# Kernel tuning notes

Measured on AMD Instinct MI355X. Metric: run time of the kernel, lower is better.

## Reference

```python
import jax, jax.numpy as jnp
import numpy as np

B, S, E, H = 2, 2048, 1024, 16
D = E // H  # head_dim = 64


def setup_inputs() -> dict:
    key = jax.random.key(0)
    ks = jax.random.split(key, 11)
    s = 1.0 / np.sqrt(E)
    return {
        "query": jax.random.normal(ks[0], (B, S, E), jnp.float32),
        "key":   jax.random.normal(ks[1], (B, S, E), jnp.float32),
        "value": jax.random.normal(ks[2], (B, S, E), jnp.float32),
        "q_w": jax.random.uniform(ks[3], (E, E), jnp.float32, -s, s),
        "q_b": jax.random.uniform(ks[4], (E,), jnp.float32, -s, s),
        "k_w": jax.random.uniform(ks[5], (E, E), jnp.float32, -s, s),
        "k_b": jax.random.uniform(ks[6], (E,), jnp.float32, -s, s),
        "v_w": jax.random.uniform(ks[7], (E, E), jnp.float32, -s, s),
        "v_b": jax.random.uniform(ks[8], (E,), jnp.float32, -s, s),
        "o_w": jax.random.uniform(ks[9], (E, E), jnp.float32, -s, s),
        "o_b": jax.random.uniform(ks[10], (E,), jnp.float32, -s, s),
    }


def reference(query, key, value, q_w, q_b, k_w, k_b, v_w, v_b, o_w, o_b):
    b, sq, _ = query.shape
    sk = key.shape[1]
    # linear projections (torch Linear: x @ W.T + b)
    Q = (query @ q_w.T + q_b).reshape(b, sq, H, D).transpose(0, 2, 1, 3)  # b h sq d
    K = (key   @ k_w.T + k_b).reshape(b, sk, H, D).transpose(0, 2, 1, 3)
    V = (value @ v_w.T + v_b).reshape(b, sk, H, D).transpose(0, 2, 1, 3)
    scores = jnp.einsum("bhqd,bhkd->bhqk", Q, K) / jnp.sqrt(jnp.float32(D))
    attn = jax.nn.softmax(scores, axis=-1)
    out = jnp.einsum("bhqk,bhkd->bhqd", attn, V)  # b h sq d
    out = out.transpose(0, 2, 1, 3).reshape(b, sq, E)
    return out @ o_w.T + o_b
```

## Files before the change

kernel.cpp:

```cpp
#include <hip/hip_runtime.h>
#include <stdint.h>

typedef __bf16 bf16x8 __attribute__((ext_vector_type(8)));
typedef short short8 __attribute__((ext_vector_type(8)));
typedef float f32x4 __attribute__((ext_vector_type(4)));
typedef float f32x16 __attribute__((ext_vector_type(16)));
typedef unsigned short u16;
typedef unsigned int u32;

#define MROWS 4096
#define EDIM  1024
#define SQ    2048
#define DH    64

#if __has_builtin(__builtin_amdgcn_exp2f)
#define EXP2(x) __builtin_amdgcn_exp2f(x)
#else
#define EXP2(x) exp2f(x)
#endif

__device__ __forceinline__ u16 f2bf(float f) {
  unsigned u = __builtin_bit_cast(unsigned, f);
  return (u16)((u + 0x7FFFu + ((u >> 16) & 1u)) >> 16);
}

__device__ __forceinline__ u32 cvtpk_bf16(float lo, float hi) {
  u32 r;
  asm("v_cvt_pk_bf16_f32 %0, %1, %2" : "=v"(r) : "v"(lo), "v"(hi));
  return r;
}
__device__ __forceinline__ void swap32(u32& a, u32& b) {
  asm("v_permlane32_swap_b32 %0, %1" : "+v"(a), "+v"(b));
}

__global__ __launch_bounds__(256) void cvt7_kernel(
    const float* __restrict__ s0, const float* __restrict__ s1,
    const float* __restrict__ s2, const float* __restrict__ s3,
    const float* __restrict__ s4, const float* __restrict__ s5,
    const float* __restrict__ s6,
    u16* __restrict__ d0, u16* __restrict__ d1, u16* __restrict__ d2,
    u16* __restrict__ d3, u16* __restrict__ d4, u16* __restrict__ d5,
    u16* __restrict__ d6, int nact, int nw) {
  const float* s; u16* d; int n;
  switch (blockIdx.y) {
    case 0: s = s0; d = d0; n = nact; break;
    case 1: s = s1; d = d1; n = nact; break;
    case 2: s = s2; d = d2; n = nact; break;
    case 3: s = s3; d = d3; n = nw; break;
    case 4: s = s4; d = d4; n = nw; break;
    case 5: s = s5; d = d5; n = nw; break;
    default: s = s6; d = d6; n = nw; break;
  }
  int i = (blockIdx.x * 256 + threadIdx.x) * 8;
  if (i >= n) return;
  float4 a = *(const float4*)(s + i);
  float4 b = *(const float4*)(s + i + 4);
  short8 r;
  r[0] = (short)f2bf(a.x); r[1] = (short)f2bf(a.y);
  r[2] = (short)f2bf(a.z); r[3] = (short)f2bf(a.w);
  r[4] = (short)f2bf(b.x); r[5] = (short)f2bf(b.y);
  r[6] = (short)f2bf(b.z); r[7] = (short)f2bf(b.w);
  *(short8*)(d + i) = r;
}

template <int OUT_F32>
__device__ __forceinline__ void gemm_core(
    const u16* __restrict__ A, const u16* __restrict__ W,
    const float* __restrict__ bias, void* __restrict__ C,
    int m0, int n0, u16* As, u16* Bs) {
  const int tid = threadIdx.x, lane = tid & 63, w = tid >> 6;
  const int r = lane & 15, g = lane >> 4;
  const int wr = w >> 1, wc = w & 1;
  f32x4 acc[4][4] = {};

  for (int kt = 0; kt < 32; ++kt) {
    const int k0 = kt * 32;
    __syncthreads();
#pragma unroll
    for (int i = 0; i < 2; ++i) {
      int c = i * 256 + tid;
      int row = c >> 2, ko = (c & 3) * 8;
      __builtin_amdgcn_global_load_lds(
          (const __attribute__((address_space(1))) void*)(A + (size_t)(m0 + row) * EDIM + k0 + ko),
          (__attribute__((address_space(3))) void*)(As + (i * 256 + w * 64) * 8), 16, 0, 0);
      __builtin_amdgcn_global_load_lds(
          (const __attribute__((address_space(1))) void*)(W + (size_t)(n0 + row) * EDIM + k0 + ko),
          (__attribute__((address_space(3))) void*)(Bs + (i * 256 + w * 64) * 8), 16, 0, 0);
    }
    __syncthreads();
    bf16x8 af[4], bfv[4];
#pragma unroll
    for (int i = 0; i < 4; ++i) {
      af[i]  = *(const bf16x8*)&As[(wr * 64 + i * 16 + r) * 32 + g * 8];
      bfv[i] = *(const bf16x8*)&Bs[(wc * 64 + i * 16 + r) * 32 + g * 8];
    }
#pragma unroll
    for (int mi = 0; mi < 4; ++mi)
#pragma unroll
      for (int ni = 0; ni < 4; ++ni)
        acc[mi][ni] = __builtin_amdgcn_mfma_f32_16x16x32_bf16(af[mi], bfv[ni], acc[mi][ni], 0, 0, 0);
  }
#pragma unroll
  for (int ni = 0; ni < 4; ++ni) {
    const int col = n0 + wc * 64 + ni * 16 + r;
    const float bv = bias[col];
#pragma unroll
    for (int mi = 0; mi < 4; ++mi) {
#pragma unroll
      for (int rr = 0; rr < 4; ++rr) {
        const int rowm = m0 + wr * 64 + mi * 16 + g * 4 + rr;
        float v = acc[mi][ni][rr] + bv;
        if (OUT_F32) ((float*)C)[(size_t)rowm * EDIM + col] = v;
        else ((u16*)C)[(size_t)rowm * EDIM + col] = f2bf(v);
      }
    }
  }
}

__global__ __launch_bounds__(256) void gemm_qkv(
    const u16* __restrict__ X0, const u16* __restrict__ X1, const u16* __restrict__ X2,
    const u16* __restrict__ W0, const u16* __restrict__ W1, const u16* __restrict__ W2,
    const float* __restrict__ b0, const float* __restrict__ b1, const float* __restrict__ b2,
    u16* __restrict__ C0, u16* __restrict__ C1, u16* __restrict__ C2) {
  __shared__ u16 As[128 * 32];
  __shared__ u16 Bs[128 * 32];
  const u16 *A, *W; const float* bias; u16* C;
  switch (blockIdx.z) {
    case 0: A = X0; W = W0; bias = b0; C = C0; break;
    case 1: A = X1; W = W1; bias = b1; C = C1; break;
    default: A = X2; W = W2; bias = b2; C = C2; break;
  }
  gemm_core<0>(A, W, bias, C, blockIdx.y * 128, blockIdx.x * 128, As, Bs);
}

__global__ __launch_bounds__(256) void gemm_oproj(
    const u16* __restrict__ A, const u16* __restrict__ W,
    const float* __restrict__ bias, float* __restrict__ C) {
  __shared__ u16 As[128 * 32];
  __shared__ u16 Bs[128 * 32];
  gemm_core<1>(A, W, bias, C, blockIdx.y * 128, blockIdx.x * 128, As, Bs);
}

__device__ __forceinline__ void k_stage(const u16* __restrict__ Kg, int kt, int tid,
                                        int w, u16* kb) {
#pragma unroll
  for (int ri = 0; ri < 2; ++ri) {
    int idx = ri * 256 + tid, row = idx >> 3, sl = idx & 7;
    __builtin_amdgcn_global_load_lds(
        (const __attribute__((address_space(1))) void*)(
            Kg + (size_t)(kt * 64 + row) * EDIM + ((sl ^ (row & 7)) * 8)),
        (__attribute__((address_space(3))) void*)(kb + (ri * 256 + w * 64) * 8), 16, 0, 0);
  }
}

__device__ __forceinline__ void v_issue(const u16* __restrict__ Vg, int kt, int tid,
                                        u32* vdw) {
  const int vd0 = (tid & 31) * 2, kvc = tid >> 5;
#pragma unroll
  for (int j = 0; j < 8; ++j)
    vdw[j] = *(const u32*)(Vg + (size_t)(kt * 64 + kvc * 8 + j) * EDIM + vd0);
}

__device__ __forceinline__ void v_write(u16* vt, int tid, const u32* vdw) {
  const int vd0 = (tid & 31) * 2, kvc = tid >> 5;
  union { u32 u[4]; short8 s; } lo8, hi8;
#pragma unroll
  for (int i = 0; i < 4; ++i) {
    lo8.u[i] = (vdw[2 * i] & 0xFFFFu) | (vdw[2 * i + 1] << 16);
    hi8.u[i] = (vdw[2 * i] >> 16) | (vdw[2 * i + 1] & 0xFFFF0000u);
  }
  const int sl = kvc ^ (vd0 & 7);
  *(short8*)&vt[vd0 * 64 + sl * 8] = lo8.s;
  *(short8*)&vt[(vd0 + 1) * 64 + (sl ^ 1) * 8] = hi8.s;
}

#define CE_CONST 0.18033688011112042f

__device__ __forceinline__ void qk_step(f32x16 (&st)[2], const u16* kb,
                                        const bf16x8 (&qf)[4], const int (&colA)[4],
                                        int lq) {
  __builtin_amdgcn_s_setprio(1);
#pragma unroll
  for (int t = 0; t < 2; ++t) {
    f32x16 z = {};
#pragma unroll
    for (int f = 0; f < 4; ++f) {
      const bf16x8 ka = *(const bf16x8*)&kb[(t * 32 + lq) * 64 + colA[f]];
      z = __builtin_amdgcn_mfma_f32_32x32x16_bf16(ka, qf[f], z, 0, 0, 0);
    }
    st[t] = z;
  }
  __builtin_amdgcn_s_setprio(0);
}

__device__ __forceinline__ void softmax_pb(f32x16 (&st)[2], float& m, float& l,
                                           f32x16 (&accO)[2], bf16x8 (&pb)[4]) {
  float vm = fmaxf(st[0][0], st[0][1]);
#pragma unroll
  for (int t = 0; t < 2; ++t)
#pragma unroll
    for (int rr = (t == 0 ? 2 : 0); rr < 16; ++rr) vm = fmaxf(vm, st[t][rr]);
  vm = fmaxf(vm, __shfl_xor(vm, 32));
  if (!__all(vm <= m + 8.0f)) {
    const float mn = fmaxf(m, vm);
    const float scl = EXP2((m - mn) * CE_CONST);
    m = mn;
    l *= scl;
#pragma unroll
    for (int dt = 0; dt < 2; ++dt)
#pragma unroll
      for (int rr = 0; rr < 16; ++rr) accO[dt][rr] *= scl;
  }
  const float mc = m * CE_CONST;
  float ts = 0.f;
#pragma unroll
  for (int t = 0; t < 2; ++t)
#pragma unroll
    for (int rr = 0; rr < 16; ++rr) {
      float pv = EXP2(st[t][rr] * CE_CONST - mc);
      st[t][rr] = pv;
      ts += pv;
    }
  ts += __shfl_xor(ts, 32);
  l += ts;
#pragma unroll
  for (int t = 0; t < 2; ++t)
#pragma unroll
    for (int kh = 0; kh < 2; ++kh) {
      const int rb = kh * 8;
      u32 a0 = cvtpk_bf16(st[t][rb + 0], st[t][rb + 1]);
      u32 b0 = cvtpk_bf16(st[t][rb + 4], st[t][rb + 5]);
      swap32(a0, b0);
      u32 a1 = cvtpk_bf16(st[t][rb + 2], st[t][rb + 3]);
      u32 b1 = cvtpk_bf16(st[t][rb + 6], st[t][rb + 7]);
      swap32(a1, b1);
      union { u32 u[4]; bf16x8 v; } pu;
      pu.u[0] = a0; pu.u[1] = a1; pu.u[2] = b0; pu.u[3] = b1;
      pb[t * 2 + kh] = pu.v;
    }
}

__device__ __forceinline__ void pv_step(f32x16 (&accO)[2], const bf16x8 (&pb)[4],
                                        const u16* vt, const int (&colA)[4], int lq) {
  __builtin_amdgcn_s_setprio(1);
#pragma unroll
  for (int dt = 0; dt < 2; ++dt)
#pragma unroll
    for (int ks = 0; ks < 4; ++ks) {
      const bf16x8 va = *(const bf16x8*)&vt[(dt * 32 + lq) * 64 + colA[ks]];
      accO[dt] = __builtin_amdgcn_mfma_f32_32x32x16_bf16(va, pb[ks], accO[dt], 0, 0, 0);
    }
  __builtin_amdgcn_s_setprio(0);
}

__global__ __launch_bounds__(256) void attn2_kernel(
    const u16* __restrict__ Q, const u16* __restrict__ K,
    const u16* __restrict__ V, u16* __restrict__ O) {
  __shared__ __align__(16) u16 KB[2][64 * 64];
  __shared__ __align__(16) u16 VT[3][64 * 64];
  const int tid = threadIdx.x, lane = tid & 63, w = tid >> 6;
  const int lq = lane & 31, hi = lane >> 5;
  const int bid = blockIdx.x;
  const int b2 = (bid & 7) * 64 + (bid >> 3);
  const int qb = b2 & 15, bh = b2 >> 4;
  const int b = bh >> 4, h = bh & 15;
  const u16* Qg = Q + (size_t)b * SQ * EDIM + h * DH;
  const u16* Kg = K + (size_t)b * SQ * EDIM + h * DH;
  const u16* Vg = V + (size_t)b * SQ * EDIM + h * DH;
  const int q0 = qb * 128 + w * 32;

  bf16x8 qf[4];
#pragma unroll
  for (int f = 0; f < 4; ++f)
    qf[f] = *(const bf16x8*)(Qg + (size_t)(q0 + lq) * EDIM + f * 16 + hi * 8);

  const int swz = (lq & 7) << 4;
  int colA[4];
#pragma unroll
  for (int f = 0; f < 4; ++f) colA[f] = ((f * 32 + hi * 16) ^ swz) >> 1;

  f32x16 accO[2] = {};
  f32x16 stA[2], stB[2];
  bf16x8 pb[4];
  float m = -3e38f, l = 0.f;
  u32 vdw[8];

  k_stage(Kg, 0, tid, w, KB[0]);
  v_issue(Vg, 0, tid, vdw);
  v_write(VT[0], tid, vdw);
  __syncthreads();
  k_stage(Kg, 1, tid, w, KB[1]);
  v_issue(Vg, 1, tid, vdw);
  qk_step(stA, KB[0], qf, colA, lq);
  v_write(VT[1], tid, vdw);
  __syncthreads();

#define ATTN_BODY(T, SP, SN)                                                  \
  {                                                                           \
    if ((T) < 31) { k_stage(Kg, (T) + 1, tid, w, KB[((T) + 1) & 1]);          \
                    v_issue(Vg, (T) + 1, tid, vdw); }                         \
    qk_step(SN, KB[(T) & 1], qf, colA, lq);                                   \
    softmax_pb(SP, m, l, accO, pb);                                           \
    pv_step(accO, pb, VT[((T) - 1) % 3], colA, lq);                           \
    if ((T) < 31) v_write(VT[((T) + 1) % 3], tid, vdw);                       \
    __syncthreads();                                                          \
  }

  for (int t = 1; t < 31; t += 2) {
    ATTN_BODY(t, stA, stB);
    ATTN_BODY(t + 1, stB, stA);
  }
  ATTN_BODY(31, stA, stB);
#undef ATTN_BODY

  softmax_pb(stB, m, l, accO, pb);
  pv_step(accO, pb, VT[31 % 3], colA, lq);

  const float rinv = 1.0f / l;
  u16* Ost = (u16*)KB;
#pragma unroll
  for (int dt = 0; dt < 2; ++dt)
#pragma unroll
    for (int rr = 0; rr < 16; ++rr) {
      const int d = dt * 32 + (rr & 3) + 8 * (rr >> 2) + 4 * hi;
      Ost[w * 2048 + lq * 64 + (d ^ ((lq & 7) << 3))] = f2bf(accO[dt][rr] * rinv);
    }
  __syncthreads();
#pragma unroll
  for (int ri = 0; ri < 4; ++ri) {
    const int idx = ri * 256 + tid;
    const int w2 = idx >> 8, q = (idx >> 3) & 31, c = idx & 7;
    short8 o = *(const short8*)&Ost[w2 * 2048 + q * 64 + ((c ^ (q & 7)) * 8)];
    *(short8*)(O + (size_t)(b * SQ + qb * 128 + w2 * 32 + q) * EDIM + h * DH + c * 8) = o;
  }
}

extern "C" void kernel_launch(void* const* d_in, const int* in_sizes, int n_in,
                              void* d_out, int out_size, void* d_ws, size_t ws_size,
                              hipStream_t stream) {
  (void)in_sizes; (void)n_in; (void)out_size; (void)ws_size;
  const float* query = (const float*)d_in[0];
  const float* key   = (const float*)d_in[1];
  const float* value = (const float*)d_in[2];
  const float* q_w = (const float*)d_in[3];
  const float* q_b = (const float*)d_in[4];
  const float* k_w = (const float*)d_in[5];
  const float* k_b = (const float*)d_in[6];
  const float* v_w = (const float*)d_in[7];
  const float* v_b = (const float*)d_in[8];
  const float* o_w = (const float*)d_in[9];
  const float* o_b = (const float*)d_in[10];

  u16* ws = (u16*)d_ws;
  const size_t NX = (size_t)MROWS * EDIM;
  const size_t NW = (size_t)EDIM * EDIM;
  u16* Xq = ws;
  u16* Xk = Xq + NX;
  u16* Xv = Xk + NX;
  u16* Wq = Xv + NX;
  u16* Wk = Wq + NW;
  u16* Wv = Wk + NW;
  u16* Wo = Wv + NW;
  u16* Qp = Wo + NW;
  u16* Kp = Qp + NX;
  u16* Vp = Kp + NX;
  u16* At = Xq;

  cvt7_kernel<<<dim3((int)(NX / 8 / 256), 7), 256, 0, stream>>>(
      query, key, value, q_w, k_w, v_w, o_w,
      Xq, Xk, Xv, Wq, Wk, Wv, Wo, (int)NX, (int)NW);

  gemm_qkv<<<dim3(8, 32, 3), 256, 0, stream>>>(
      Xq, Xk, Xv, Wq, Wk, Wv, q_b, k_b, v_b, Qp, Kp, Vp);

  attn2_kernel<<<512, 256, 0, stream>>>(Qp, Kp, Vp, At);

  gemm_oproj<<<dim3(8, 32), 256, 0, stream>>>(At, Wo, o_b, (float*)d_out);
}
```

Baseline: 137.1 us.

## Fuse fp32-to-bf16 conversion into projection GEMMs and drop separate convert kernel

Removes the standalone conversion pass that cast inputs and weights to bf16. The QKV and output projection GEMMs now stage fp32 tiles into LDS with an XOR swizzle and pack to bf16 in registers before the MFMA. This saves one launch and a full write and re-read of the converted activations. In exchange each GEMM moves twice the global and LDS bytes per tile and spends extra VALU on packing. The output projection also switches to 128x64 tiles, doubling its grid.

After: 152.9 us. 11.5% more time.

```diff
diff --git a/kernel.cpp b/kernel.cpp
--- a/kernel.cpp
+++ b/kernel.cpp
@@ -33,112 +33,143 @@
   asm("v_permlane32_swap_b32 %0, %1" : "+v"(a), "+v"(b));
 }
 
-__global__ __launch_bounds__(256) void cvt7_kernel(
-    const float* __restrict__ s0, const float* __restrict__ s1,
-    const float* __restrict__ s2, const float* __restrict__ s3,
-    const float* __restrict__ s4, const float* __restrict__ s5,
-    const float* __restrict__ s6,
-    u16* __restrict__ d0, u16* __restrict__ d1, u16* __restrict__ d2,
-    u16* __restrict__ d3, u16* __restrict__ d4, u16* __restrict__ d5,
-    u16* __restrict__ d6, int nact, int nw) {
-  const float* s; u16* d; int n;
-  switch (blockIdx.y) {
-    case 0: s = s0; d = d0; n = nact; break;
-    case 1: s = s1; d = d1; n = nact; break;
-    case 2: s = s2; d = d2; n = nact; break;
-    case 3: s = s3; d = d3; n = nw; break;
-    case 4: s = s4; d = d4; n = nw; break;
-    case 5: s = s5; d = d5; n = nw; break;
-    default: s = s6; d = d6; n = nw; break;
-  }
-  int i = (blockIdx.x * 256 + threadIdx.x) * 8;
-  if (i >= n) return;
-  float4 a = *(const float4*)(s + i);
-  float4 b = *(const float4*)(s + i + 4);
-  short8 r;
-  r[0] = (short)f2bf(a.x); r[1] = (short)f2bf(a.y);
-  r[2] = (short)f2bf(a.z); r[3] = (short)f2bf(a.w);
-  r[4] = (short)f2bf(b.x); r[5] = (short)f2bf(b.y);
-  r[6] = (short)f2bf(b.z); r[7] = (short)f2bf(b.w);
-  *(short8*)(d + i) = r;
-}
-
-template <int OUT_F32>
-__device__ __forceinline__ void gemm_core(
-    const u16* __restrict__ A, const u16* __restrict__ W,
-    const float* __restrict__ bias, void* __restrict__ C,
-    int m0, int n0, u16* As, u16* Bs) {
-  const int tid = threadIdx.x, lane = tid & 63, w = tid >> 6;
-  const int r = lane & 15, g = lane >> 4;
-  const int wr = w >> 1, wc = w & 1;
-  f32x4 acc[4][4] = {};
-
-  for (int kt = 0; kt < 32; ++kt) {
-    const int k0 = kt * 32;
-    __syncthreads();
-#pragma unroll
-    for (int i = 0; i < 2; ++i) {
-      int c = i * 256 + tid;
-      int row = c >> 2, ko = (c & 3) * 8;
-      __builtin_amdgcn_global_load_lds(
-          (const __attribute__((address_space(1))) void*)(A + (size_t)(m0 + row) * EDIM + k0 + ko),
-          (__attribute__((address_space(3))) void*)(As + (i * 256 + w * 64) * 8), 16, 0, 0);
-      __builtin_amdgcn_global_load_lds(
-          (const __attribute__((address_space(1))) void*)(W + (size_t)(n0 + row) * EDIM + k0 + ko),
-          (__attribute__((address_space(3))) void*)(Bs + (i * 256 + w * 64) * 8), 16, 0, 0);
-    }
-    __syncthreads();
-    bf16x8 af[4], bfv[4];
-#pragma unroll
-    for (int i = 0; i < 4; ++i) {
-      af[i]  = *(const bf16x8*)&As[(wr * 64 + i * 16 + r) * 32 + g * 8];
-      bfv[i] = *(const bf16x8*)&Bs[(wc * 64 + i * 16 + r) * 32 + g * 8];
-    }
-#pragma unroll
-    for (int mi = 0; mi < 4; ++mi)
-#pragma unroll
-      for (int ni = 0; ni < 4; ++ni)
-        acc[mi][ni] = __builtin_amdgcn_mfma_f32_16x16x32_bf16(af[mi], bfv[ni], acc[mi][ni], 0, 0, 0);
-  }
-#pragma unroll
-  for (int ni = 0; ni < 4; ++ni) {
-    const int col = n0 + wc * 64 + ni * 16 + r;
-    const float bv = bias[col];
-#pragma unroll
-    for (int mi = 0; mi < 4; ++mi) {
-#pragma unroll
-      for (int rr = 0; rr < 4; ++rr) {
-        const int rowm = m0 + wr * 64 + mi * 16 + g * 4 + rr;
-        float v = acc[mi][ni][rr] + bv;
-        if (OUT_F32) ((float*)C)[(size_t)rowm * EDIM + col] = v;
-        else ((u16*)C)[(size_t)rowm * EDIM + col] = f2bf(v);
-      }
-    }
-  }
-}
-
-__global__ __launch_bounds__(256) void gemm_qkv(
-    const u16* __restrict__ X0, const u16* __restrict__ X1, const u16* __restrict__ X2,
-    const u16* __restrict__ W0, const u16* __restrict__ W1, const u16* __restrict__ W2,
+__device__ __forceinline__ bf16x8 pack_bf8(f32x4 q0, f32x4 q1) {
+  union { u32 u[4]; bf16x8 v; } pu;
+  pu.u[0] = cvtpk_bf16(q0[0], q0[1]);
+  pu.u[1] = cvtpk_bf16(q0[2], q0[3]);
+  pu.u[2] = cvtpk_bf16(q1[0], q1[1]);
+  pu.u[3] = cvtpk_bf16(q1[2], q1[3]);
+  return pu.v;
+}
+
+__global__ __launch_bounds__(256) void gemm_qkv_f32(
+    const float* __restrict__ X0, const float* __restrict__ X1, const float* __restrict__ X2,
+    const float* __restrict__ W0, const float* __restrict__ W1, const float* __restrict__ W2,
     const float* __restrict__ b0, const float* __restrict__ b1, const float* __restrict__ b2,
     u16* __restrict__ C0, u16* __restrict__ C1, u16* __restrict__ C2) {
-  __shared__ u16 As[128 * 32];
-  __shared__ u16 Bs[128 * 32];
-  const u16 *A, *W; const float* bias; u16* C;
+  __shared__ __align__(16) float As[128 * 32];
+  __shared__ __align__(16) float Bs[128 * 32];
+  const float *A, *W, *bias; u16* C;
   switch (blockIdx.z) {
     case 0: A = X0; W = W0; bias = b0; C = C0; break;
     case 1: A = X1; W = W1; bias = b1; C = C1; break;
     default: A = X2; W = W2; bias = b2; C = C2; break;
   }
-  gemm_core<0>(A, W, bias, C, blockIdx.y * 128, blockIdx.x * 128, As, Bs);
+  const int tid = threadIdx.x, lane = tid & 63, w = tid >> 6;
+  const int r = lane & 15, g = lane >> 4;
+  const int m0 = blockIdx.y * 128, n0 = blockIdx.x * 128;
+  const int wr = w >> 1, wc = w & 1;
+  f32x4 acc[4][4] = {};
+
+  for (int kt = 0; kt < 32; ++kt) {
+    const int k0 = kt * 32;
+    __syncthreads();
+#pragma unroll
+    for (int i = 0; i < 4; ++i) {
+      const int c = i * 256 + tid;
+      const int row = c >> 3, sl = c & 7;
+      const int ko = k0 + ((sl ^ (row & 7)) * 4);
+      __builtin_amdgcn_global_load_lds(
+          (const __attribute__((address_space(1))) void*)(A + (size_t)(m0 + row) * EDIM + ko),
+          (__attribute__((address_space(3))) void*)(As + (i * 256 + w * 64) * 4), 16, 0, 0);
+      __builtin_amdgcn_global_load_lds(
+          (const __attribute__((address_space(1))) void*)(W + (size_t)(n0 + row) * EDIM + ko),
+          (__attribute__((address_space(3))) void*)(Bs + (i * 256 + w * 64) * 4), 16, 0, 0);
+    }
+    __syncthreads();
+    bf16x8 af[4], bfv[4];
+#pragma unroll
+    for (int i = 0; i < 4; ++i) {
+      const int ra = wr * 64 + i * 16 + r;
+      const int rb = wc * 64 + i * 16 + r;
+      f32x4 a0 = *(const f32x4*)&As[ra * 32 + (((g * 2 + 0) ^ (ra & 7)) * 4)];
+      f32x4 a1 = *(const f32x4*)&As[ra * 32 + (((g * 2 + 1) ^ (ra & 7)) * 4)];
+      af[i] = pack_bf8(a0, a1);
+      f32x4 w0 = *(const f32x4*)&Bs[rb * 32 + (((g * 2 + 0) ^ (rb & 7)) * 4)];
+      f32x4 w1 = *(const f32x4*)&Bs[rb * 32 + (((g * 2 + 1) ^ (rb & 7)) * 4)];
+      bfv[i] = pack_bf8(w0, w1);
+    }
+#pragma unroll
+    for (int mi = 0; mi < 4; ++mi)
+#pragma unroll
+      for (int ni = 0; ni < 4; ++ni)
+        acc[mi][ni] = __builtin_amdgcn_mfma_f32_16x16x32_bf16(af[mi], bfv[ni], acc[mi][ni], 0, 0, 0);
+  }
+#pragma unroll
+  for (int ni = 0; ni < 4; ++ni) {
+    const int col = n0 + wc * 64 + ni * 16 + r;
+    const float bv = bias[col];
+#pragma unroll
+    for (int mi = 0; mi < 4; ++mi)
+#pragma unroll
+      for (int rr = 0; rr < 4; ++rr) {
+        const int rowm = m0 + wr * 64 + mi * 16 + g * 4 + rr;
+        C[(size_t)rowm * EDIM + col] = f2bf(acc[mi][ni][rr] + bv);
+      }
+  }
 }
 
 __global__ __launch_bounds__(256) void gemm_oproj(
-    const u16* __restrict__ A, const u16* __restrict__ W,
+    const u16* __restrict__ A, const float* __restrict__ W,
     const float* __restrict__ bias, float* __restrict__ C) {
-  __shared__ u16 As[128 * 32];
-  __shared__ u16 Bs[128 * 32];
-  gemm_core<1>(A, W, bias, C, blockIdx.y * 128, blockIdx.x * 128, As, Bs);
+  __shared__ __align__(16) u16 As[128 * 32];
+  __shared__ __align__(16) float Bs[64 * 32];
+  const int tid = threadIdx.x, lane = tid & 63, w = tid >> 6;
+  const int r = lane & 15, g = lane >> 4;
+  const int m0 = blockIdx.y * 128, n0 = blockIdx.x * 64;
+  const int wr = w >> 1, wc = w & 1;
+  f32x4 acc[4][2] = {};
+
+  for (int kt = 0; kt < 32; ++kt) {
+    const int k0 = kt * 32;
+    __syncthreads();
+#pragma unroll
+    for (int i = 0; i < 2; ++i) {
+      const int c = i * 256 + tid;
+      const int row = c >> 2, ko = (c & 3) * 8;
+      __builtin_amdgcn_global_load_lds(
+          (const __attribute__((address_space(1))) void*)(A + (size_t)(m0 + row) * EDIM + k0 + ko),
+          (__attribute__((address_space(3))) void*)(As + (i * 256 + w * 64) * 8), 16, 0, 0);
+    }
+#pragma unroll
+    for (int i = 0; i < 2; ++i) {
+      const int c = i * 256 + tid;
+      const int row = c >> 3, sl = c & 7;
+      const int ko = k0 + ((sl ^ (row & 7)) * 4);
+      __builtin_amdgcn_global_load_lds(
+          (const __attribute__((address_space(1))) void*)(W + (size_t)(n0 + row) * EDIM + ko),
+          (__attribute__((address_space(3))) void*)(Bs + (i * 256 + w * 64) * 4), 16, 0, 0);
+    }
+    __syncthreads();
+    bf16x8 af[4], bfv[2];
+#pragma unroll
+    for (int i = 0; i < 4; ++i)
+      af[i] = *(const bf16x8*)&As[(wr * 64 + i * 16 + r) * 32 + g * 8];
+#pragma unroll
+    for (int i = 0; i < 2; ++i) {
+      const int rb = wc * 32 + i * 16 + r;
+      f32x4 w0 = *(const f32x4*)&Bs[rb * 32 + (((g * 2 + 0) ^ (rb & 7)) * 4)];
+      f32x4 w1 = *(const f32x4*)&Bs[rb * 32 + (((g * 2 + 1) ^ (rb & 7)) * 4)];
+      bfv[i] = pack_bf8(w0, w1);
+    }
+#pragma unroll
+    for (int mi = 0; mi < 4; ++mi)
+#pragma unroll
+      for (int ni = 0; ni < 2; ++ni)
+        acc[mi][ni] = __builtin_amdgcn_mfma_f32_16x16x32_bf16(af[mi], bfv[ni], acc[mi][ni], 0, 0, 0);
+  }
+#pragma unroll
+  for (int ni = 0; ni < 2; ++ni) {
+    const int col = n0 + wc * 32 + ni * 16 + r;
+    const float bv = bias[col];
+#pragma unroll
+    for (int mi = 0; mi < 4; ++mi)
+#pragma unroll
+      for (int rr = 0; rr < 4; ++rr) {
+        const int rowm = m0 + wr * 64 + mi * 16 + g * 4 + rr;
+        C[(size_t)rowm * EDIM + col] = acc[mi][ni][rr] + bv;
+      }
+  }
 }
 
 __device__ __forceinline__ void k_stage(const u16* __restrict__ Kg, int kt, int tid,
@@ -353,27 +384,15 @@
 
   u16* ws = (u16*)d_ws;
   const size_t NX = (size_t)MROWS * EDIM;
-  const size_t NW = (size_t)EDIM * EDIM;
-  u16* Xq = ws;
-  u16* Xk = Xq + NX;
-  u16* Xv = Xk + NX;
-  u16* Wq = Xv + NX;
-  u16* Wk = Wq + NW;
-  u16* Wv = Wk + NW;
-  u16* Wo = Wv + NW;
-  u16* Qp = Wo + NW;
+  u16* Qp = ws;
   u16* Kp = Qp + NX;
   u16* Vp = Kp + NX;
-  u16* At = Xq;
-
-  cvt7_kernel<<<dim3((int)(NX / 8 / 256), 7), 256, 0, stream>>>(
-      query, key, value, q_w, k_w, v_w, o_w,
-      Xq, Xk, Xv, Wq, Wk, Wv, Wo, (int)NX, (int)NW);
-
-  gemm_qkv<<<dim3(8, 32, 3), 256, 0, stream>>>(
-      Xq, Xk, Xv, Wq, Wk, Wv, q_b, k_b, v_b, Qp, Kp, Vp);
+  u16* At = Vp + NX;
+
+  gemm_qkv_f32<<<dim3(8, 32, 3), 256, 0, stream>>>(
+      query, key, value, q_w, k_w, v_w, q_b, k_b, v_b, Qp, Kp, Vp);
 
   attn2_kernel<<<512, 256, 0, stream>>>(Qp, Kp, Vp, At);
 
-  gemm_oproj<<<dim3(8, 32), 256, 0, stream>>>(At, Wo, o_b, (float*)d_out);
-}
+  gemm_oproj<<<dim3(16, 32), 256, 0, stream>>>(At, o_w, o_b, (float*)d_out);
+}
```
